# Performance work log

Measured on AMD Instinct MI355X. Metric: run time of the kernel, lower is better.

## Reference

```python
import jax, jax.numpy as jnp
import numpy as np
import math

B, S, D, H = 4, 2048, 1024, 16
HD = D // H


def setup_inputs() -> dict:
    key = jax.random.key(0)
    ks = jax.random.split(key, 12)
    sc = 1.0 / math.sqrt(D)
    inp = {
        "query": jax.random.normal(ks[0], (B, S, D), jnp.float32),
        "key": jax.random.normal(ks[1], (B, S, D), jnp.float32),
        "value": jax.random.normal(ks[2], (B, S, D), jnp.float32),
        "mask": jnp.tril(jnp.ones((S, S), jnp.bool_))[None, None],  # [1,1,S,S] causal
        "wq": jax.random.normal(ks[3], (D, D), jnp.float32) * sc,
        "bq": jax.random.normal(ks[4], (D,), jnp.float32) * sc,
        "wk": jax.random.normal(ks[5], (D, D), jnp.float32) * sc,
        "bk": jax.random.normal(ks[6], (D,), jnp.float32) * sc,
        "wv": jax.random.normal(ks[7], (D, D), jnp.float32) * sc,
        "bv": jax.random.normal(ks[8], (D,), jnp.float32) * sc,
        "wo": jax.random.normal(ks[9], (D, D), jnp.float32) * sc,
        "bo": jax.random.normal(ks[10], (D,), jnp.float32) * sc,
    }
    return inp


def reference(query, key, value, mask, wq, bq, wk, bk, wv, bv, wo, bo):
    # QKV projections (torch Linear: x @ W.T + b)
    q = query @ wq.T + bq
    k = key @ wk.T + bk
    v = value @ wv.T + bv
    # [B,S,D] -> [B,H,S,HD]
    q = q.reshape(B, S, H, HD).transpose(0, 2, 1, 3)
    k = k.reshape(B, S, H, HD).transpose(0, 2, 1, 3)
    v = v.reshape(B, S, H, HD).transpose(0, 2, 1, 3)
    scores = jnp.einsum("bhqd,bhkd->bhqk", q, k) / math.sqrt(HD)
    scores = jnp.where(mask, scores, -jnp.inf)
    weights = jax.nn.softmax(scores, axis=-1)
    attn = jnp.einsum("bhqk,bhkd->bhqd", weights, v)
    attn = attn.transpose(0, 2, 1, 3).reshape(B, S, D)
    return attn @ wo.T + bo
```

## Files before the change

### kernel.cpp

```cpp
#include <hip/hip_runtime.h>
#include <hip/hip_bf16.h>

#define B_  4
#define S_  2048
#define D_  1024
#define H_  16
#define HD_ 64
#define M_  (B_ * S_)

typedef __bf16 bf16x8 __attribute__((ext_vector_type(8)));
typedef float  f32x4  __attribute__((ext_vector_type(4)));
typedef float  f32x16 __attribute__((ext_vector_type(16)));
typedef unsigned int   u32x4 __attribute__((ext_vector_type(4)));
typedef unsigned short u16x8 __attribute__((ext_vector_type(8)));

typedef __attribute__((address_space(1))) const void gv_t;
typedef __attribute__((address_space(3))) void lv_t;

__device__ inline bf16x8 cvt8(float4 a, float4 b) {
    bf16x8 r;
    r[0] = (__bf16)a.x; r[1] = (__bf16)a.y; r[2] = (__bf16)a.z; r[3] = (__bf16)a.w;
    r[4] = (__bf16)b.x; r[5] = (__bf16)b.y; r[6] = (__bf16)b.z; r[7] = (__bf16)b.w;
    return r;
}

__device__ __forceinline__ unsigned pk2(float lo, float hi) {
    unsigned short a = __builtin_bit_cast(unsigned short, (__bf16)lo);
    unsigned short b = __builtin_bit_cast(unsigned short, (__bf16)hi);
    return (unsigned)a | ((unsigned)b << 16);
}

__global__ __launch_bounds__(256) void cvt_all(
    const float* __restrict__ q, const float* __restrict__ k,
    const float* __restrict__ v, const float* __restrict__ wq,
    const float* __restrict__ wk, const float* __restrict__ wv,
    const float* __restrict__ wo, __bf16* __restrict__ xq,
    __bf16* __restrict__ xk, __bf16* __restrict__ xv,
    __bf16* __restrict__ bwq, __bf16* __restrict__ bwk,
    __bf16* __restrict__ bwv, __bf16* __restrict__ bwo) {
    const size_t NI = 8388608, NW = 1048576;
    const size_t total = 3 * NI + 4 * NW;
    const size_t step = (size_t)gridDim.x * 256 * 8;
    for (size_t e = ((size_t)blockIdx.x * 256 + threadIdx.x) * 8; e < total;
         e += step) {
        const float* s; __bf16* d;
        if (e < NI)            { s = q + e;           d = xq + e; }
        else if (e < 2 * NI)   { s = k + (e - NI);    d = xk + (e - NI); }
        else if (e < 3 * NI)   { s = v + (e - 2*NI);  d = xv + (e - 2*NI); }
        else {
            size_t r = e - 3 * NI;
            if (r < NW)        { s = wq + r;          d = bwq + r; }
            else if (r < 2*NW) { s = wk + (r - NW);   d = bwk + (r - NW); }
            else if (r < 3*NW) { s = wv + (r - 2*NW); d = bwv + (r - 2*NW); }
            else               { s = wo + (r - 3*NW); d = bwo + (r - 3*NW); }
        }
        *(bf16x8*)d = cvt8(*(const float4*)s, *(const float4*)(s + 4));
    }
}

template <int OUT_MODE>
__device__ __forceinline__ void gemm_body(
    const __bf16* __restrict__ A, const __bf16* __restrict__ Wb,
    const float* __restrict__ bias, void* __restrict__ Yv, float out_scale,
    __bf16* As, __bf16* Bs) {
    const int K = 1024, N = 1024;
    const int m0 = blockIdx.x * 128, n0 = blockIdx.y * 128;
    const int tid = threadIdx.x;
    const int w = tid >> 6, lane = tid & 63;
    const int wr = (w >> 1) * 64, wc = (w & 1) * 64;
    const int l15 = lane & 15, hi4 = lane >> 4;

    f32x4 acc[4][4] = {};

    const int srow8 = tid >> 3;
    const int sblk  = tid & 7;

    for (int kb = 0; kb < K; kb += 64) {
#pragma unroll
        for (int c = 0; c < 4; ++c) {
            int row = c * 32 + srow8;
            int soff = ((sblk ^ (row & 7)) << 4);
            const char* sa = (const char*)(A + (size_t)(m0 + row) * K + kb) + soff;
            __builtin_amdgcn_global_load_lds(
                (gv_t*)sa, (lv_t*)((char*)As + c * 4096 + tid * 16), 16, 0, 0);
            const char* sb = (const char*)(Wb + (size_t)(n0 + row) * K + kb) + soff;
            __builtin_amdgcn_global_load_lds(
                (gv_t*)sb, (lv_t*)((char*)Bs + c * 4096 + tid * 16), 16, 0, 0);
        }
        __syncthreads();
#pragma unroll
        for (int kh = 0; kh < 2; ++kh) {
            bf16x8 af[4], bfr[4];
            const int blk = kh * 4 + hi4;
#pragma unroll
            for (int m = 0; m < 4; ++m) {
                int row = wr + m * 16 + l15;
                af[m] = *(const bf16x8*)((const char*)As + row * 128 +
                                         ((blk ^ (row & 7)) << 4));
            }
#pragma unroll
            for (int n = 0; n < 4; ++n) {
                int row = wc + n * 16 + l15;
                bfr[n] = *(const bf16x8*)((const char*)Bs + row * 128 +
                                          ((blk ^ (row & 7)) << 4));
            }
#pragma unroll
            for (int m = 0; m < 4; ++m)
#pragma unroll
                for (int n = 0; n < 4; ++n)
                    acc[m][n] = __builtin_amdgcn_mfma_f32_16x16x32_bf16(
                        af[m], bfr[n], acc[m][n], 0, 0, 0);
        }
        __syncthreads();
    }

#pragma unroll
    for (int n = 0; n < 4; ++n) {
        int col = n0 + wc + n * 16 + l15;
        float bb = bias[col];
#pragma unroll
        for (int m = 0; m < 4; ++m) {
            int rowb = m0 + wr + m * 16 + hi4 * 4;
#pragma unroll
            for (int r = 0; r < 4; ++r) {
                float v = (acc[m][n][r] + bb) * out_scale;
                int row = rowb + r;
                if (OUT_MODE == 0) {
                    ((float*)Yv)[(size_t)row * N + col] = v;
                } else {
                    int b = row >> 11, s = row & (S_ - 1);
                    int h = col >> 6, hd = col & (HD_ - 1);
                    ((__bf16*)Yv)[(((size_t)(b * H_ + h)) * S_ + s) * HD_ + hd] =
                        (__bf16)v;
                }
            }
        }
    }
}

__global__ __launch_bounds__(256) void gemm_qkv(
    const __bf16* __restrict__ xq, const __bf16* __restrict__ xk,
    const __bf16* __restrict__ xv, const __bf16* __restrict__ wqb,
    const __bf16* __restrict__ wkb, const __bf16* __restrict__ wvb,
    const float* __restrict__ bq, const float* __restrict__ bk,
    const float* __restrict__ bv, __bf16* __restrict__ oq,
    __bf16* __restrict__ ok, __bf16* __restrict__ ov, float qsc) {
    __shared__ __align__(16) __bf16 As[128 * 64];
    __shared__ __align__(16) __bf16 Bs[128 * 64];
    const __bf16 *A, *Wb; const float* bias; __bf16* Y; float sc;
    if (blockIdx.z == 0)      { A = xq; Wb = wqb; bias = bq; Y = oq; sc = qsc; }
    else if (blockIdx.z == 1) { A = xk; Wb = wkb; bias = bk; Y = ok; sc = 1.f; }
    else                      { A = xv; Wb = wvb; bias = bv; Y = ov; sc = 1.f; }
    gemm_body<1>(A, Wb, bias, (void*)Y, sc, As, Bs);
}

__global__ __launch_bounds__(256) void gemm_o(
    const __bf16* __restrict__ A, const __bf16* __restrict__ Wb,
    const float* __restrict__ bias, float* __restrict__ Y) {
    __shared__ __align__(16) __bf16 As[128 * 64];
    __shared__ __align__(16) __bf16 Bs[128 * 64];
    gemm_body<0>(A, Wb, bias, (void*)Y, 1.0f, As, Bs);
}

__device__ __forceinline__ void stage_k256(__bf16* kbuf, const __bf16* Kh,
                                           int k0, int tid) {
#pragma unroll
    for (int c = 0; c < 2; ++c) {
        int row = c * 32 + (tid >> 3);
        int blk = (tid & 7) ^ (row & 7);
        const char* src = (const char*)(Kh + (size_t)(k0 + row) * HD_) + blk * 16;
        __builtin_amdgcn_global_load_lds(
            (gv_t*)src, (lv_t*)((char*)kbuf + c * 4096 + tid * 16), 16, 0, 0);
    }
}

__device__ __forceinline__ u16x8 load_v8(const __bf16* Vh, int k0, int vrg,
                                         int vcol) {
    u16x8 r;
#pragma unroll
    for (int j = 0; j < 8; ++j)
        r[j] = *(const unsigned short*)(Vh + (size_t)(k0 + vrg * 8 + j) * HD_ + vcol);
    return r;
}

__device__ __forceinline__ void store_vt(__bf16* vt, u16x8 a, int vcol, int blk) {
    int byt = vcol * 128 + ((blk ^ (vcol & 7)) << 4);
    *(u16x8*)((char*)vt + byt) = a;
}

__global__ __launch_bounds__(256, 2) void attn_fwd(
    const __bf16* __restrict__ Q, const __bf16* __restrict__ K,
    const __bf16* __restrict__ V, __bf16* __restrict__ O) {
    __shared__ __align__(16) __bf16 Kb[3][64 * 64];
    __shared__ __align__(16) __bf16 Vt[2][64 * 64];
    const int bh = blockIdx.x;
    const int qt = 15 - blockIdx.y;
    const int tid = threadIdx.x, w = tid >> 6, lane = tid & 63;
    const int l31 = lane & 31, hi = lane >> 5;
    const size_t base = (size_t)bh * S_ * HD_;
    const __bf16* Qh = Q + base;
    const __bf16* Kh = K + base;
    const __bf16* Vh = V + base;
    const int b = bh >> 4, h = bh & 15;
    const int vcol = tid & 63, vrg = tid >> 6;

    const u32x4 onew = {0x3F803F80u, 0x3F803F80u, 0x3F803F80u, 0x3F803F80u};
    const bf16x8 onef = __builtin_bit_cast(bf16x8, onew);

    const int qb0 = qt * 128;
    const int NS = 2 * qt + 2;
    const int qw0 = qb0 + w * 32;
    const int qrow = qw0 + l31;

    bf16x8 qf[4];
#pragma unroll
    for (int sl = 0; sl < 4; ++sl)
        qf[sl] = *(const bf16x8*)(Qh + (size_t)qrow * HD_ + sl * 16 + hi * 8);

    f32x16 accO[2] = {};
    f32x16 accL = {};

    u16x8 va = load_v8(Vh, 0, vrg, vcol);
    u16x8 vb = load_v8(Vh, 32, vrg, vcol);
    __builtin_amdgcn_sched_barrier(0);
    stage_k256(&Kb[0][0], Kh, 0, tid);
    stage_k256(&Kb[1][0], Kh, 64, tid);
    __builtin_amdgcn_sched_barrier(0);
    asm volatile("s_waitcnt vmcnt(2)" ::: "memory");
    __builtin_amdgcn_sched_barrier(0);
    store_vt(&Vt[0][0], va, vcol, vrg);
    store_vt(&Vt[0][0], vb, vcol, vrg + 4);
    asm volatile("s_waitcnt lgkmcnt(0)" ::: "memory");
    __builtin_amdgcn_sched_barrier(0);
    __builtin_amdgcn_s_barrier();
    __builtin_amdgcn_sched_barrier(0);

    for (int s = 0; s < NS; ++s) {
        const int k0 = s * 64;
        const int tV = (s + 1 < NS) ? s + 1 : NS - 1;
        const int tK = (s + 2 < NS) ? s + 2 : NS - 1;
        u16x8 nva = load_v8(Vh, tV * 64, vrg, vcol);
        u16x8 nvb = load_v8(Vh, tV * 64 + 32, vrg, vcol);
        __builtin_amdgcn_sched_barrier(0);
        stage_k256(&Kb[(s + 2) % 3][0], Kh, tK * 64, tid);
        __builtin_amdgcn_sched_barrier(0);

        const bool active = (k0 <= qw0 + 31);
        if (active) {
            const char* kbuf = (const char*)&Kb[s % 3][0];
            const char* vbuf = (const char*)&Vt[s & 1][0];
            f32x16 sc[2] = {};
            __builtin_amdgcn_s_setprio(1);
#pragma unroll
            for (int sub = 0; sub < 2; ++sub)
#pragma unroll
                for (int sl = 0; sl < 4; ++sl) {
                    int row = sub * 32 + l31;
                    int byt = row * 128 + (((2 * sl + hi) ^ (row & 7)) << 4);
                    bf16x8 kf = *(const bf16x8*)(kbuf + byt);
                    sc[sub] = __builtin_amdgcn_mfma_f32_32x32x16_bf16(
                        kf, qf[sl], sc[sub], 0, 0, 0);
                }
            __builtin_amdgcn_s_setprio(0);
            if (k0 + 64 > qw0) {
#pragma unroll
                for (int sub = 0; sub < 2; ++sub)
#pragma unroll
                    for (int r = 0; r < 16; ++r) {
                        int k = k0 + 32 * sub + (r & 3) + 8 * (r >> 2) + 4 * hi;
                        if (k > qrow) sc[sub][r] = -3.0e38f;
                    }
            }
#pragma unroll
            for (int sub = 0; sub < 2; ++sub)
#pragma unroll
                for (int r = 0; r < 16; ++r)
                    sc[sub][r] = __builtin_amdgcn_exp2f(sc[sub][r]);
            bf16x8 pa[4];
#pragma unroll
            for (int sl = 0; sl < 4; ++sl) {
                const int sub = sl >> 1, rb = 8 * (sl & 1);
                u32x4 wds = {pk2(sc[sub][rb + 0], sc[sub][rb + 1]),
                             pk2(sc[sub][rb + 2], sc[sub][rb + 3]),
                             pk2(sc[sub][rb + 4], sc[sub][rb + 5]),
                             pk2(sc[sub][rb + 6], sc[sub][rb + 7])};
                pa[sl] = __builtin_bit_cast(bf16x8, wds);
            }
            __builtin_amdgcn_s_setprio(1);
#pragma unroll
            for (int t = 0; t < 2; ++t)
#pragma unroll
                for (int sl = 0; sl < 4; ++sl) {
                    int row = t * 32 + l31;
                    const char* vbp = vbuf + row * 128 + hi * 8;
                    uint2 lo = *(const uint2*)(vbp + (((2 * sl) ^ (row & 7)) << 4));
                    uint2 hw = *(const uint2*)(vbp + (((2 * sl + 1) ^ (row & 7)) << 4));
                    u32x4 vv = {lo.x, lo.y, hw.x, hw.y};
                    bf16x8 vf = __builtin_bit_cast(bf16x8, vv);
                    accO[t] = __builtin_amdgcn_mfma_f32_32x32x16_bf16(
                        vf, pa[sl], accO[t], 0, 0, 0);
                }
#pragma unroll
            for (int sl = 0; sl < 4; ++sl)
                accL = __builtin_amdgcn_mfma_f32_32x32x16_bf16(
                    onef, pa[sl], accL, 0, 0, 0);
            __builtin_amdgcn_s_setprio(0);
        }
        asm volatile("s_waitcnt vmcnt(2)" ::: "memory");
        __builtin_amdgcn_sched_barrier(0);
        store_vt(&Vt[(s + 1) & 1][0], nva, vcol, vrg);
        store_vt(&Vt[(s + 1) & 1][0], nvb, vcol, vrg + 4);
        asm volatile("s_waitcnt lgkmcnt(0)" ::: "memory");
        __builtin_amdgcn_sched_barrier(0);
        __builtin_amdgcn_s_barrier();
        __builtin_amdgcn_sched_barrier(0);
    }

    float inv = 1.0f / accL[0];
    __bf16* orow = O + ((size_t)b * S_ + qrow) * D_ + h * HD_;
#pragma unroll
    for (int t = 0; t < 2; ++t)
#pragma unroll
        for (int g = 0; g < 4; ++g) {
            unsigned w0 = pk2(accO[t][4 * g + 0] * inv, accO[t][4 * g + 1] * inv);
            unsigned w1 = pk2(accO[t][4 * g + 2] * inv, accO[t][4 * g + 3] * inv);
            uint2 u = {w0, w1};
            *(uint2*)(orow + t * 32 + g * 8 + hi * 4) = u;
        }
}

extern "C" void kernel_launch(void* const* d_in, const int* in_sizes, int n_in,
                              void* d_out, int out_size, void* d_ws, size_t ws_size,
                              hipStream_t stream) {
    const float* query = (const float*)d_in[0];
    const float* key_  = (const float*)d_in[1];
    const float* value = (const float*)d_in[2];
    const float* wq = (const float*)d_in[4];
    const float* bq = (const float*)d_in[5];
    const float* wk = (const float*)d_in[6];
    const float* bk = (const float*)d_in[7];
    const float* wv = (const float*)d_in[8];
    const float* bv = (const float*)d_in[9];
    const float* wo = (const float*)d_in[10];
    const float* bo = (const float*)d_in[11];
    float* out = (float*)d_out;

    const float QSC = 0.125f * 1.44269504088896341f;

    const size_t SZ = (size_t)M_ * D_ * 2;
    const size_t WB = (size_t)D_ * D_ * 2;
    char* wsb = (char*)d_ws;
    __bf16* qws = (__bf16*)(wsb + 0 * SZ);
    __bf16* kws = (__bf16*)(wsb + 1 * SZ);
    __bf16* vws = (__bf16*)(wsb + 2 * SZ);
    __bf16* aws = (__bf16*)(wsb + 3 * SZ);
    __bf16* xq  = (__bf16*)(wsb + 4 * SZ);
    __bf16* xk  = (__bf16*)(wsb + 5 * SZ);
    __bf16* xv  = (__bf16*)(wsb + 6 * SZ);
    __bf16* bwq = (__bf16*)(wsb + 7 * SZ);
    __bf16* bwk = (__bf16*)(wsb + 7 * SZ + 1 * WB);
    __bf16* bwv = (__bf16*)(wsb + 7 * SZ + 2 * WB);
    __bf16* bwo = (__bf16*)(wsb + 7 * SZ + 3 * WB);

    dim3 bb(256);
    hipLaunchKernelGGL(cvt_all, dim3(2048), bb, 0, stream,
                       query, key_, value, wq, wk, wv, wo,
                       xq, xk, xv, bwq, bwk, bwv, bwo);
    hipLaunchKernelGGL(gemm_qkv, dim3(M_ / 128, D_ / 128, 3), bb, 0, stream,
                       xq, xk, xv, bwq, bwk, bwv, bq, bk, bv,
                       qws, kws, vws, QSC);
    hipLaunchKernelGGL(attn_fwd, dim3(B_ * H_, 16), bb, 0, stream,
                       qws, kws, vws, aws);
    hipLaunchKernelGGL(gemm_o, dim3(M_ / 128, D_ / 128), bb, 0, stream,
                       aws, bwo, bo, out);
}
```

Before: 181.7 us.

## Fuse fp32-to-bf16 activation conversion into QKV projection GEMM loads

Removes the separate conversion pass over the query, key and value activations. The QKV GEMM now stages fp32 A tiles into LDS through direct global-to-LDS loads with a 16-block XOR swizzle, then converts them to bf16 in registers before the MFMAs. The standalone conversion kernel now handles only the four weight matrices. This avoids writing and re-reading about 150 MB of bf16 intermediates, but doubles LDS use and global reads for the A tile in the GEMM, since each A tile is re-read once per N-block.

```diff
diff --git a/kernel.cpp b/kernel.cpp
--- a/kernel.cpp
+++ b/kernel.cpp
@@ -30,39 +30,129 @@
     return (unsigned)a | ((unsigned)b << 16);
 }
 
-__global__ __launch_bounds__(256) void cvt_all(
-    const float* __restrict__ q, const float* __restrict__ k,
-    const float* __restrict__ v, const float* __restrict__ wq,
-    const float* __restrict__ wk, const float* __restrict__ wv,
-    const float* __restrict__ wo, __bf16* __restrict__ xq,
-    __bf16* __restrict__ xk, __bf16* __restrict__ xv,
-    __bf16* __restrict__ bwq, __bf16* __restrict__ bwk,
-    __bf16* __restrict__ bwv, __bf16* __restrict__ bwo) {
-    const size_t NI = 8388608, NW = 1048576;
-    const size_t total = 3 * NI + 4 * NW;
+__global__ __launch_bounds__(256) void cvt_w(
+    const float* __restrict__ wq, const float* __restrict__ wk,
+    const float* __restrict__ wv, const float* __restrict__ wo,
+    __bf16* __restrict__ oq, __bf16* __restrict__ ok,
+    __bf16* __restrict__ ov, __bf16* __restrict__ oo) {
+    const size_t NW = 1048576;
     const size_t step = (size_t)gridDim.x * 256 * 8;
-    for (size_t e = ((size_t)blockIdx.x * 256 + threadIdx.x) * 8; e < total;
+    for (size_t e = ((size_t)blockIdx.x * 256 + threadIdx.x) * 8; e < 4 * NW;
          e += step) {
         const float* s; __bf16* d;
-        if (e < NI)            { s = q + e;           d = xq + e; }
-        else if (e < 2 * NI)   { s = k + (e - NI);    d = xk + (e - NI); }
-        else if (e < 3 * NI)   { s = v + (e - 2*NI);  d = xv + (e - 2*NI); }
-        else {
-            size_t r = e - 3 * NI;
-            if (r < NW)        { s = wq + r;          d = bwq + r; }
-            else if (r < 2*NW) { s = wk + (r - NW);   d = bwk + (r - NW); }
-            else if (r < 3*NW) { s = wv + (r - 2*NW); d = bwv + (r - 2*NW); }
-            else               { s = wo + (r - 3*NW); d = bwo + (r - 3*NW); }
-        }
+        if (e < NW)            { s = wq + e;          d = oq + e; }
+        else if (e < 2 * NW)   { s = wk + (e - NW);   d = ok + (e - NW); }
+        else if (e < 3 * NW)   { s = wv + (e - 2*NW); d = ov + (e - 2*NW); }
+        else                   { s = wo + (e - 3*NW); d = oo + (e - 3*NW); }
         *(bf16x8*)d = cvt8(*(const float4*)s, *(const float4*)(s + 4));
     }
 }
 
-template <int OUT_MODE>
-__device__ __forceinline__ void gemm_body(
+__device__ __forceinline__ void gemm_body_f32A(
+    const float* __restrict__ A, const __bf16* __restrict__ Wb,
+    const float* __restrict__ bias, __bf16* __restrict__ Y, float out_scale,
+    float* Asf, __bf16* Bs) {
+    const int K = 1024;
+    const int m0 = blockIdx.x * 128, n0 = blockIdx.y * 128;
+    const int tid = threadIdx.x;
+    const int w = tid >> 6, lane = tid & 63;
+    const int wr = (w >> 1) * 64, wc = (w & 1) * 64;
+    const int l15 = lane & 15, hi4 = lane >> 4;
+
+    f32x4 acc[4][4] = {};
+
+    const int srow8  = tid >> 3;
+    const int sblk8  = tid & 7;
+    const int srow16 = tid >> 4;
+    const int sblk16 = tid & 15;
+
+    for (int kb = 0; kb < K; kb += 64) {
+#pragma unroll
+        for (int c = 0; c < 4; ++c) {
+            int row = c * 32 + srow8;
+            int soff = ((sblk8 ^ (row & 7)) << 4);
+            const char* sb = (const char*)(Wb + (size_t)(n0 + row) * K + kb) + soff;
+            __builtin_amdgcn_global_load_lds(
+                (gv_t*)sb, (lv_t*)((char*)Bs + c * 4096 + tid * 16), 16, 0, 0);
+        }
+#pragma unroll
+        for (int c = 0; c < 8; ++c) {
+            int row = c * 16 + srow16;
+            int soff = ((sblk16 ^ (row & 15)) << 4);
+            const char* sa = (const char*)(A + (size_t)(m0 + row) * K + kb) + soff;
+            __builtin_amdgcn_global_load_lds(
+                (gv_t*)sa, (lv_t*)((char*)Asf + c * 4096 + tid * 16), 16, 0, 0);
+        }
+        __syncthreads();
+#pragma unroll
+        for (int kh = 0; kh < 2; ++kh) {
+            bf16x8 af[4], bfr[4];
+#pragma unroll
+            for (int m = 0; m < 4; ++m) {
+                int row = wr + m * 16 + l15;
+                const char* base = (const char*)Asf + row * 256;
+                int b0 = kh * 8 + hi4 * 2;
+                float4 a0 = *(const float4*)(base + ((b0 ^ (row & 15)) << 4));
+                float4 a1 = *(const float4*)(base + (((b0 + 1) ^ (row & 15)) << 4));
+                af[m] = cvt8(a0, a1);
+            }
+            const int blk = kh * 4 + hi4;
+#pragma unroll
+            for (int n = 0; n < 4; ++n) {
+                int row = wc + n * 16 + l15;
+                bfr[n] = *(const bf16x8*)((const char*)Bs + row * 128 +
+                                          ((blk ^ (row & 7)) << 4));
+            }
+#pragma unroll
+            for (int m = 0; m < 4; ++m)
+#pragma unroll
+                for (int n = 0; n < 4; ++n)
+                    acc[m][n] = __builtin_amdgcn_mfma_f32_16x16x32_bf16(
+                        af[m], bfr[n], acc[m][n], 0, 0, 0);
+        }
+        __syncthreads();
+    }
+
+#pragma unroll
+    for (int n = 0; n < 4; ++n) {
+        int col = n0 + wc + n * 16 + l15;
+        float bb = bias[col];
+#pragma unroll
+        for (int m = 0; m < 4; ++m) {
+            int rowb = m0 + wr + m * 16 + hi4 * 4;
+#pragma unroll
+            for (int r = 0; r < 4; ++r) {
+                float v = (acc[m][n][r] + bb) * out_scale;
+                int row = rowb + r;
+                int b = row >> 11, s = row & (S_ - 1);
+                int h = col >> 6, hd = col & (HD_ - 1);
+                Y[(((size_t)(b * H_ + h)) * S_ + s) * HD_ + hd] = (__bf16)v;
+            }
+        }
+    }
+}
+
+__global__ __launch_bounds__(256) void gemm_qkv(
+    const float* __restrict__ q, const float* __restrict__ k,
+    const float* __restrict__ v, const __bf16* __restrict__ wqb,
+    const __bf16* __restrict__ wkb, const __bf16* __restrict__ wvb,
+    const float* __restrict__ bq, const float* __restrict__ bk,
+    const float* __restrict__ bv, __bf16* __restrict__ oq,
+    __bf16* __restrict__ ok, __bf16* __restrict__ ov, float qsc) {
+    __shared__ __align__(16) float  Asf[128 * 64];
+    __shared__ __align__(16) __bf16 Bs[128 * 64];
+    const float *A; const __bf16 *Wb; const float* bias; __bf16* Y; float sc;
+    if (blockIdx.z == 0)      { A = q; Wb = wqb; bias = bq; Y = oq; sc = qsc; }
+    else if (blockIdx.z == 1) { A = k; Wb = wkb; bias = bk; Y = ok; sc = 1.f; }
+    else                      { A = v; Wb = wvb; bias = bv; Y = ov; sc = 1.f; }
+    gemm_body_f32A(A, Wb, bias, Y, sc, Asf, Bs);
+}
+
+__global__ __launch_bounds__(256) void gemm_o(
     const __bf16* __restrict__ A, const __bf16* __restrict__ Wb,
-    const float* __restrict__ bias, void* __restrict__ Yv, float out_scale,
-    __bf16* As, __bf16* Bs) {
+    const float* __restrict__ bias, float* __restrict__ Y) {
+    __shared__ __align__(16) __bf16 As[128 * 64];
+    __shared__ __align__(16) __bf16 Bs[128 * 64];
     const int K = 1024, N = 1024;
     const int m0 = blockIdx.x * 128, n0 = blockIdx.y * 128;
     const int tid = threadIdx.x;
@@ -122,44 +212,10 @@
         for (int m = 0; m < 4; ++m) {
             int rowb = m0 + wr + m * 16 + hi4 * 4;
 #pragma unroll
-            for (int r = 0; r < 4; ++r) {
-                float v = (acc[m][n][r] + bb) * out_scale;
-                int row = rowb + r;
-                if (OUT_MODE == 0) {
-                    ((float*)Yv)[(size_t)row * N + col] = v;
-                } else {
-                    int b = row >> 11, s = row & (S_ - 1);
-                    int h = col >> 6, hd = col & (HD_ - 1);
-                    ((__bf16*)Yv)[(((size_t)(b * H_ + h)) * S_ + s) * HD_ + hd] =
-                        (__bf16)v;
-                }
-            }
-        }
-    }
-}
-
-__global__ __launch_bounds__(256) void gemm_qkv(
-    const __bf16* __restrict__ xq, const __bf16* __restrict__ xk,
-    const __bf16* __restrict__ xv, const __bf16* __restrict__ wqb,
-    const __bf16* __restrict__ wkb, const __bf16* __restrict__ wvb,
-    const float* __restrict__ bq, const float* __restrict__ bk,
-    const float* __restrict__ bv, __bf16* __restrict__ oq,
-    __bf16* __restrict__ ok, __bf16* __restrict__ ov, float qsc) {
-    __shared__ __align__(16) __bf16 As[128 * 64];
-    __shared__ __align__(16) __bf16 Bs[128 * 64];
-    const __bf16 *A, *Wb; const float* bias; __bf16* Y; float sc;
-    if (blockIdx.z == 0)      { A = xq; Wb = wqb; bias = bq; Y = oq; sc = qsc; }
-    else if (blockIdx.z == 1) { A = xk; Wb = wkb; bias = bk; Y = ok; sc = 1.f; }
-    else                      { A = xv; Wb = wvb; bias = bv; Y = ov; sc = 1.f; }
-    gemm_body<1>(A, Wb, bias, (void*)Y, sc, As, Bs);
-}
-
-__global__ __launch_bounds__(256) void gemm_o(
-    const __bf16* __restrict__ A, const __bf16* __restrict__ Wb,
-    const float* __restrict__ bias, float* __restrict__ Y) {
-    __shared__ __align__(16) __bf16 As[128 * 64];
-    __shared__ __align__(16) __bf16 Bs[128 * 64];
-    gemm_body<0>(A, Wb, bias, (void*)Y, 1.0f, As, Bs);
+            for (int r = 0; r < 4; ++r)
+                Y[(size_t)(rowb + r) * N + col] = acc[m][n][r] + bb;
+        }
+    }
 }
 
 __device__ __forceinline__ void stage_k256(__bf16* kbuf, const __bf16* Kh,
@@ -354,20 +410,16 @@
     __bf16* kws = (__bf16*)(wsb + 1 * SZ);
     __bf16* vws = (__bf16*)(wsb + 2 * SZ);
     __bf16* aws = (__bf16*)(wsb + 3 * SZ);
-    __bf16* xq  = (__bf16*)(wsb + 4 * SZ);
-    __bf16* xk  = (__bf16*)(wsb + 5 * SZ);
-    __bf16* xv  = (__bf16*)(wsb + 6 * SZ);
-    __bf16* bwq = (__bf16*)(wsb + 7 * SZ);
-    __bf16* bwk = (__bf16*)(wsb + 7 * SZ + 1 * WB);
-    __bf16* bwv = (__bf16*)(wsb + 7 * SZ + 2 * WB);
-    __bf16* bwo = (__bf16*)(wsb + 7 * SZ + 3 * WB);
+    __bf16* bwq = (__bf16*)(wsb + 4 * SZ);
+    __bf16* bwk = (__bf16*)(wsb + 4 * SZ + 1 * WB);
+    __bf16* bwv = (__bf16*)(wsb + 4 * SZ + 2 * WB);
+    __bf16* bwo = (__bf16*)(wsb + 4 * SZ + 3 * WB);
 
     dim3 bb(256);
-    hipLaunchKernelGGL(cvt_all, dim3(2048), bb, 0, stream,
-                       query, key_, value, wq, wk, wv, wo,
-                       xq, xk, xv, bwq, bwk, bwv, bwo);
+    hipLaunchKernelGGL(cvt_w, dim3(512), bb, 0, stream,
+                       wq, wk, wv, wo, bwq, bwk, bwv, bwo);
     hipLaunchKernelGGL(gemm_qkv, dim3(M_ / 128, D_ / 128, 3), bb, 0, stream,
-                       xq, xk, xv, bwq, bwk, bwv, bq, bk, bv,
+                       query, key_, value, bwq, bwk, bwv, bq, bk, bv,
                        qws, kws, vws, QSC);
     hipLaunchKernelGGL(attn_fwd, dim3(B_ * H_, 16), bb, 0, stream,
                        qws, kws, vws, aws);
```

After: 174.3 us (median of 3 runs). 4.1% less time.
